# Optimization experiments

Hardware: AMD Instinct MI355X
Metric: run time of the kernel (lower is better)

The kernel has to match this reference:

```python
import jax, jax.numpy as jnp
import numpy as np

D_MODEL = 1024
NUM_HEADS = 16
D_K = D_MODEL // NUM_HEADS


def setup_inputs() -> dict:
    key = jax.random.key(0)
    ks = jax.random.split(key, 7)
    B, S = 4, 2048
    lim = float(np.sqrt(6.0 / (D_MODEL + D_MODEL)))  # xavier uniform
    x = jax.random.normal(ks[0], (B, S, D_MODEL), dtype=jnp.float32)
    w_q = jax.random.uniform(ks[1], (D_MODEL, D_MODEL), jnp.float32, -lim, lim)
    w_k = jax.random.uniform(ks[2], (D_MODEL, D_MODEL), jnp.float32, -lim, lim)
    w_v = jax.random.uniform(ks[3], (D_MODEL, D_MODEL), jnp.float32, -lim, lim)
    w_o = jax.random.uniform(ks[4], (D_MODEL, D_MODEL), jnp.float32, -lim, lim)
    b_o = jnp.zeros((D_MODEL,), jnp.float32)
    ln_g = jnp.ones((D_MODEL,), jnp.float32)
    ln_b = jnp.zeros((D_MODEL,), jnp.float32)
    return {"x": x, "w_q": w_q, "w_k": w_k, "w_v": w_v, "w_o": w_o,
            "b_o": b_o, "ln_g": ln_g, "ln_b": ln_b}


def _layer_norm(y, g, b, eps=1e-5):
    mu = jnp.mean(y, axis=-1, keepdims=True)
    var = jnp.var(y, axis=-1, keepdims=True)
    return (y - mu) * jax.lax.rsqrt(var + eps) * g + b


def reference(x, w_q, w_k, w_v, w_o, b_o, ln_g, ln_b):
    B, S, D = x.shape
    # Linear weights stored torch-style [out, in]: y = x @ W^T
    def proj(w):
        return jnp.einsum('bsd,ed->bse', x, w).reshape(B, S, NUM_HEADS, D_K).transpose(0, 2, 1, 3)
    Q, K, V = proj(w_q), proj(w_k), proj(w_v)  # [B, H, S, d_k]
    scores = jnp.einsum('bhqd,bhkd->bhqk', Q, K) / jnp.sqrt(jnp.float32(D_K))
    attn = jax.nn.softmax(scores, axis=-1)  # dropout identity at eval
    out = jnp.einsum('bhqk,bhkd->bhqd', attn, V)  # [B, H, S, d_k]
    out = out.transpose(0, 2, 1, 3).reshape(B, S, D)
    out = jnp.einsum('bsd,ed->bse', out, w_o) + b_o
    return _layer_norm(x + out, ln_g, ln_b)
```

## Files before the change

### kernel.cpp

```cpp
#include <hip/hip_runtime.h>

typedef __bf16 bf16;
typedef bf16 v8bf __attribute__((ext_vector_type(8)));
typedef bf16 v4bf __attribute__((ext_vector_type(4)));
typedef float v4f __attribute__((ext_vector_type(4)));

#define GAS __attribute__((address_space(1)))
#define LAS __attribute__((address_space(3)))

constexpr int D    = 1024;
constexpr int ROWS = 8192;
constexpr int TILE = 128;
constexpr int BK   = 32;

__global__ __launch_bounds__(256) void cast_f32_bf16(
    const float* __restrict__ in, bf16* __restrict__ out, int n4)
{
    int i = blockIdx.x * 256 + threadIdx.x;
    if (i < n4) {
        float4 v = ((const float4*)in)[i];
        v4bf o;
        o[0] = (bf16)v.x; o[1] = (bf16)v.y; o[2] = (bf16)v.z; o[3] = (bf16)v.w;
        ((v4bf*)out)[i] = o;
    }
}

template<int MODE>
__global__ __launch_bounds__(256) void gemm_bt(
    const bf16* __restrict__ A,
    const bf16* __restrict__ W0, const bf16* __restrict__ W1, const bf16* __restrict__ W2,
    bf16* __restrict__ O0, bf16* __restrict__ O1, bf16* __restrict__ O2,
    float* __restrict__ Of, const float* __restrict__ bias,
    const float* __restrict__ X)
{
    __shared__ bf16 As[TILE * BK];
    __shared__ bf16 Bs[TILE * BK];

    const int tid  = threadIdx.x;
    const int lane = tid & 63;
    const int wave = tid >> 6;
    const int quad = lane >> 4;
    const int l16  = lane & 15;
    const int wm   = (wave >> 1) * 64;
    const int wn   = (wave & 1) * 64;

    const int z = blockIdx.z;
    const bf16* Bw = (MODE == 0) ? ((z == 0) ? W0 : ((z == 1) ? W1 : W2)) : W0;
    bf16*       Ob = (MODE == 0) ? ((z == 0) ? O0 : ((z == 1) ? O1 : O2)) : O0;

    const long rowA0 = (long)blockIdx.y * TILE;
    const long rowB0 = (long)blockIdx.x * TILE;

    const int stRow = wave * 16 + (lane >> 2);
    const int stCol = (lane & 3) * 8;
    const bf16* gA = A  + (rowA0 + stRow) * D + stCol;
    const bf16* gB = Bw + (rowB0 + stRow) * D + stCol;
    const int ldsOff = wave * 16 * BK;

    const v4f vzero = {0.f, 0.f, 0.f, 0.f};
    v4f acc[4][4];
    #pragma unroll
    for (int i = 0; i < 4; i++)
        #pragma unroll
        for (int j = 0; j < 4; j++) acc[i][j] = vzero;

    for (int k0 = 0; k0 < D; k0 += BK) {
        __syncthreads();
        #pragma unroll
        for (int i = 0; i < 2; ++i) {
            __builtin_amdgcn_global_load_lds((const GAS void*)(gA + (long)i * 64 * D),
                                             (LAS void*)(As + ldsOff + i * 64 * BK), 16, 0, 0);
            __builtin_amdgcn_global_load_lds((const GAS void*)(gB + (long)i * 64 * D),
                                             (LAS void*)(Bs + ldsOff + i * 64 * BK), 16, 0, 0);
        }
        gA += BK; gB += BK;
        __syncthreads();

        v8bf a[4], b[4];
        #pragma unroll
        for (int mi = 0; mi < 4; mi++)
            a[mi] = *(const v8bf*)(As + (wm + mi * 16 + l16) * BK + quad * 8);
        #pragma unroll
        for (int ni = 0; ni < 4; ni++)
            b[ni] = *(const v8bf*)(Bs + (wn + ni * 16 + l16) * BK + quad * 8);
        #pragma unroll
        for (int mi = 0; mi < 4; mi++)
            #pragma unroll
            for (int ni = 0; ni < 4; ni++)
                acc[mi][ni] = __builtin_amdgcn_mfma_f32_16x16x32_bf16(a[mi], b[ni], acc[mi][ni], 0, 0, 0);
    }

    const float qscale = 0.125f * 1.44269504f;

    if (MODE == 0 && z == 2) {
        #pragma unroll
        for (int mi = 0; mi < 4; mi++) {
            #pragma unroll
            for (int ni = 0; ni < 4; ni++) {
                const long col = rowB0 + wn + ni * 16 + l16;
                const long h_ = col >> 6, dd = col & 63;
                const long row0 = rowA0 + wm + mi * 16 + quad * 4;
                const long b_ = row0 >> 11, s0 = row0 & 2047;
                v4bf pk;
                #pragma unroll
                for (int r = 0; r < 4; r++) pk[r] = (bf16)acc[mi][ni][r];
                *(v4bf*)(Ob + ((b_ * 16 + h_) * 64 + dd) * 2048 + s0) = pk;
            }
        }
    } else {
        #pragma unroll
        for (int mi = 0; mi < 4; mi++) {
            #pragma unroll
            for (int ni = 0; ni < 4; ni++) {
                const long col = rowB0 + wn + ni * 16 + l16;
                float bv = (MODE == 1) ? bias[col] : 0.f;
                #pragma unroll
                for (int r = 0; r < 4; r++) {
                    const long row = rowA0 + wm + mi * 16 + quad * 4 + r;
                    float v = acc[mi][ni][r];
                    if (MODE == 1) Of[row * D + col] = v + bv + X[row * D + col];
                    else {
                        if (z == 0) v *= qscale;
                        Ob[row * D + col] = (bf16)v;
                    }
                }
            }
        }
    }
}

__global__ __launch_bounds__(256) void attn_kernel(
    const bf16* __restrict__ Q, const bf16* __restrict__ Kg,
    const bf16* __restrict__ VtG, bf16* __restrict__ O)
{
    const int qt = blockIdx.x, h = blockIdx.y, b = blockIdx.z;
    const int tid  = threadIdx.x;
    const int lane = tid & 63;
    const int wave = tid >> 6;
    const int quad = lane >> 4;
    const int l16  = lane & 15;

    __shared__ bf16 Kt[64 * 72];
    __shared__ bf16 Vt[64 * 72];
    __shared__ bf16 Ps[4][32 * 72];

    v8bf qB[2][2];
    #pragma unroll
    for (int qf = 0; qf < 2; qf++) {
        const long qrow = (long)(b * 2048 + qt * 128 + wave * 32 + qf * 16 + l16);
        #pragma unroll
        for (int hh = 0; hh < 2; hh++)
            qB[qf][hh] = *(const v8bf*)(Q + qrow * D + h * 64 + hh * 32 + quad * 8);
    }

    float l_acc[2] = {0.f, 0.f};
    v4f o_acc[2][4];
    const v4f vzero = {0.f, 0.f, 0.f, 0.f};
    #pragma unroll
    for (int qf = 0; qf < 2; qf++)
        #pragma unroll
        for (int nf = 0; nf < 4; nf++) o_acc[qf][nf] = vzero;

    const int sC = (tid & 7) * 8;
    const int iR = tid >> 3;
    const bf16* kBase = Kg + (long)b * 2048 * D + h * 64 + sC;
    const bf16* vBase = VtG + (long)(b * 16 + h) * 64 * 2048 + sC;

    v8bf kpre[2], vpre[2];
    #pragma unroll
    for (int rep = 0; rep < 2; ++rep) {
        const int i = rep * 32 + iR;
        kpre[rep] = *(const v8bf*)(kBase + (long)i * D);
        vpre[rep] = *(const v8bf*)(vBase + (long)i * 2048);
    }

    for (int kt = 0; kt < 32; ++kt) {
        __syncthreads();
        #pragma unroll
        for (int rep = 0; rep < 2; ++rep) {
            const int i = rep * 32 + iR;
            *(v8bf*)(Kt + i * 72 + sC) = kpre[rep];
            *(v8bf*)(Vt + i * 72 + sC) = vpre[rep];
        }
        __syncthreads();

        if (kt + 1 < 32) {
            #pragma unroll
            for (int rep = 0; rep < 2; ++rep) {
                const int i = rep * 32 + iR;
                kpre[rep] = *(const v8bf*)(kBase + (long)((kt + 1) * 64 + i) * D);
                vpre[rep] = *(const v8bf*)(vBase + (long)i * 2048 + (kt + 1) * 64);
            }
        }

        v4f st[4][2];
        #pragma unroll
        for (int kf = 0; kf < 4; kf++) {
            v8bf kA0 = *(const v8bf*)(Kt + (kf * 16 + l16) * 72 + quad * 8);
            v8bf kA1 = *(const v8bf*)(Kt + (kf * 16 + l16) * 72 + 32 + quad * 8);
            #pragma unroll
            for (int qf = 0; qf < 2; qf++) {
                v4f t = vzero;
                t = __builtin_amdgcn_mfma_f32_16x16x32_bf16(kA0, qB[qf][0], t, 0, 0, 0);
                t = __builtin_amdgcn_mfma_f32_16x16x32_bf16(kA1, qB[qf][1], t, 0, 0, 0);
                st[kf][qf] = t;
            }
        }

        #pragma unroll
        for (int qf = 0; qf < 2; qf++)
            #pragma unroll
            for (int kf = 0; kf < 4; kf++) {
                v4bf pk;
                #pragma unroll
                for (int r = 0; r < 4; r++) {
                    float p = exp2f(st[kf][qf][r]);
                    l_acc[qf] += p;
                    pk[r] = (bf16)p;
                }
                *(v4bf*)(&Ps[wave][(qf * 16 + l16) * 72 + kf * 16 + quad * 4]) = pk;
            }

        #pragma unroll
        for (int ks = 0; ks < 2; ++ks) {
            v8bf vb[4];
            #pragma unroll
            for (int nf = 0; nf < 4; nf++)
                vb[nf] = *(const v8bf*)(Vt + (nf * 16 + l16) * 72 + ks * 32 + quad * 8);
            #pragma unroll
            for (int qf = 0; qf < 2; qf++) {
                v8bf pa = *(const v8bf*)(&Ps[wave][(qf * 16 + l16) * 72 + ks * 32 + quad * 8]);
                #pragma unroll
                for (int nf = 0; nf < 4; nf++)
                    o_acc[qf][nf] = __builtin_amdgcn_mfma_f32_16x16x32_bf16(pa, vb[nf], o_acc[qf][nf], 0, 0, 0);
            }
        }
    }

    #pragma unroll
    for (int qf = 0; qf < 2; qf++) {
        float l = l_acc[qf];
        l += __shfl_xor(l, 16);
        l += __shfl_xor(l, 32);
        l_acc[qf] = l;
    }

    #pragma unroll
    for (int qf = 0; qf < 2; qf++) {
        float inv[4];
        #pragma unroll
        for (int r = 0; r < 4; r++) {
            const int src = (quad << 4) | (quad * 4 + r);
            inv[r] = 1.f / __shfl(l_acc[qf], src);
        }
        const long orow = (long)(b * 2048 + qt * 128 + wave * 32 + qf * 16 + quad * 4);
        #pragma unroll
        for (int nf = 0; nf < 4; nf++)
            #pragma unroll
            for (int r = 0; r < 4; r++)
                O[(orow + r) * D + h * 64 + nf * 16 + l16] = (bf16)(o_acc[qf][nf][r] * inv[r]);
    }
}

__global__ __launch_bounds__(256) void ln_kernel(
    const float* __restrict__ g, const float* __restrict__ beta,
    float* __restrict__ out)
{
    const int row = blockIdx.x;
    const int t = threadIdx.x;
    const int lane = t & 63, wave = t >> 6;
    const long base = (long)row * D + t * 4;

    float4 yv = *(const float4*)(out + base);
    float y0 = yv.x, y1 = yv.y, y2 = yv.z, y3 = yv.w;
    float s1 = y0 + y1 + y2 + y3;
    float s2 = y0*y0 + y1*y1 + y2*y2 + y3*y3;
    #pragma unroll
    for (int off = 1; off < 64; off <<= 1) {
        s1 += __shfl_xor(s1, off);
        s2 += __shfl_xor(s2, off);
    }
    __shared__ float r1[4], r2[4];
    if (lane == 0) { r1[wave] = s1; r2[wave] = s2; }
    __syncthreads();
    float S1 = r1[0] + r1[1] + r1[2] + r1[3];
    float S2 = r2[0] + r2[1] + r2[2] + r2[3];
    float mu  = S1 * (1.f / 1024.f);
    float var = S2 * (1.f / 1024.f) - mu * mu;
    float rsd = rsqrtf(var + 1e-5f);

    float4 gv = *(const float4*)(g + t * 4);
    float4 bv = *(const float4*)(beta + t * 4);
    float4 o;
    o.x = (y0 - mu) * rsd * gv.x + bv.x;
    o.y = (y1 - mu) * rsd * gv.y + bv.y;
    o.z = (y2 - mu) * rsd * gv.z + bv.z;
    o.w = (y3 - mu) * rsd * gv.w + bv.w;
    *(float4*)(out + base) = o;
}

extern "C" void kernel_launch(void* const* d_in, const int* in_sizes, int n_in,
                              void* d_out, int out_size, void* d_ws, size_t ws_size,
                              hipStream_t stream)
{
    const float* x   = (const float*)d_in[0];
    const float* wq  = (const float*)d_in[1];
    const float* wk  = (const float*)d_in[2];
    const float* wv  = (const float*)d_in[3];
    const float* wo  = (const float*)d_in[4];
    const float* bo  = (const float*)d_in[5];
    const float* lng = (const float*)d_in[6];
    const float* lnb = (const float*)d_in[7];
    float* out = (float*)d_out;

    char* ws = (char*)d_ws;
    bf16* xb  = (bf16*)(ws);
    bf16* wqb = (bf16*)(ws + (size_t)16 * 1024 * 1024);
    bf16* wkb = wqb + 1024 * 1024;
    bf16* wvb = wkb + 1024 * 1024;
    bf16* wob = wvb + 1024 * 1024;
    bf16* Qb  = (bf16*)(ws + (size_t)24 * 1024 * 1024);
    bf16* Kb  = Qb + (size_t)ROWS * D;
    bf16* VtG = Kb + (size_t)ROWS * D;
    bf16* Ab  = VtG + (size_t)ROWS * D;

    cast_f32_bf16<<<8192, 256, 0, stream>>>(x,  xb,  ROWS * D / 4);
    cast_f32_bf16<<<1024, 256, 0, stream>>>(wq, wqb, D * D / 4);
    cast_f32_bf16<<<1024, 256, 0, stream>>>(wk, wkb, D * D / 4);
    cast_f32_bf16<<<1024, 256, 0, stream>>>(wv, wvb, D * D / 4);
    cast_f32_bf16<<<1024, 256, 0, stream>>>(wo, wob, D * D / 4);

    dim3 gqkv(D / TILE, ROWS / TILE, 3);
    gemm_bt<0><<<gqkv, 256, 0, stream>>>(xb, wqb, wkb, wvb, Qb, Kb, VtG,
                                         nullptr, nullptr, nullptr);

    attn_kernel<<<dim3(16, 16, 4), 256, 0, stream>>>(Qb, Kb, VtG, Ab);

    dim3 gout(D / TILE, ROWS / TILE, 1);
    gemm_bt<1><<<gout, 256, 0, stream>>>(Ab, wob, nullptr, nullptr,
                                         nullptr, nullptr, nullptr, out, bo, x);

    ln_kernel<<<8192, 256, 0, stream>>>(lng, lnb, out);
}
```

Before: 335.6 us.

## Merge cast kernels, double GEMM k-step to 64, simplify attention load addressing

Five separate f32-to-bf16 cast launches are merged into one kernel that picks its source and destination by index range, removing four launches. The GEMM now loads two 32-wide K slices per iteration into two LDS buffers, halving the number of barrier pairs over the K loop at the cost of twice the LDS. The attention kernel's K/V prefetch addressing is rewritten with incrementing per-lane pointers in place of recomputed indices, trimming integer address arithmetic.

Result: faster. 328.2 us (-2.2%).

```diff
diff --git a/kernel.cpp b/kernel.cpp
--- a/kernel.cpp
+++ b/kernel.cpp
@@ -11,18 +11,28 @@
 constexpr int D    = 1024;
 constexpr int ROWS = 8192;
 constexpr int TILE = 128;
-constexpr int BK   = 32;
-
-__global__ __launch_bounds__(256) void cast_f32_bf16(
-    const float* __restrict__ in, bf16* __restrict__ out, int n4)
+
+__global__ __launch_bounds__(256) void cast_all(
+    const float* __restrict__ x,
+    const float* __restrict__ wq, const float* __restrict__ wk,
+    const float* __restrict__ wv, const float* __restrict__ wo,
+    bf16* __restrict__ xb, bf16* __restrict__ wqb, bf16* __restrict__ wkb,
+    bf16* __restrict__ wvb, bf16* __restrict__ wob)
 {
     int i = blockIdx.x * 256 + threadIdx.x;
-    if (i < n4) {
-        float4 v = ((const float4*)in)[i];
-        v4bf o;
-        o[0] = (bf16)v.x; o[1] = (bf16)v.y; o[2] = (bf16)v.z; o[3] = (bf16)v.w;
-        ((v4bf*)out)[i] = o;
-    }
+    const float* src; bf16* dst; int off;
+    if (i < 2 * 1024 * 1024) { src = x; dst = xb; off = i; }
+    else {
+        int j = i - 2 * 1024 * 1024;
+        int w = j >> 18;
+        off = j & ((1 << 18) - 1);
+        src = (w == 0) ? wq : (w == 1) ? wk : (w == 2) ? wv : wo;
+        dst = (w == 0) ? wqb : (w == 1) ? wkb : (w == 2) ? wvb : wob;
+    }
+    float4 v = ((const float4*)src)[off];
+    v4bf o;
+    o[0] = (bf16)v.x; o[1] = (bf16)v.y; o[2] = (bf16)v.z; o[3] = (bf16)v.w;
+    ((v4bf*)dst)[off] = o;
 }
 
 template<int MODE>
@@ -33,8 +43,8 @@
     float* __restrict__ Of, const float* __restrict__ bias,
     const float* __restrict__ X)
 {
-    __shared__ bf16 As[TILE * BK];
-    __shared__ bf16 Bs[TILE * BK];
+    __shared__ bf16 As[2][TILE * 32];
+    __shared__ bf16 Bs[2][TILE * 32];
 
     const int tid  = threadIdx.x;
     const int lane = tid & 63;
@@ -55,7 +65,7 @@
     const int stCol = (lane & 3) * 8;
     const bf16* gA = A  + (rowA0 + stRow) * D + stCol;
     const bf16* gB = Bw + (rowB0 + stRow) * D + stCol;
-    const int ldsOff = wave * 16 * BK;
+    const int ldsOff = wave * 16 * 32;
 
     const v4f vzero = {0.f, 0.f, 0.f, 0.f};
     v4f acc[4][4];
@@ -64,30 +74,37 @@
         #pragma unroll
         for (int j = 0; j < 4; j++) acc[i][j] = vzero;
 
-    for (int k0 = 0; k0 < D; k0 += BK) {
+    for (int k0 = 0; k0 < D; k0 += 64) {
         __syncthreads();
         #pragma unroll
-        for (int i = 0; i < 2; ++i) {
-            __builtin_amdgcn_global_load_lds((const GAS void*)(gA + (long)i * 64 * D),
-                                             (LAS void*)(As + ldsOff + i * 64 * BK), 16, 0, 0);
-            __builtin_amdgcn_global_load_lds((const GAS void*)(gB + (long)i * 64 * D),
-                                             (LAS void*)(Bs + ldsOff + i * 64 * BK), 16, 0, 0);
-        }
-        gA += BK; gB += BK;
+        for (int p = 0; p < 2; ++p)
+            #pragma unroll
+            for (int i = 0; i < 2; ++i) {
+                __builtin_amdgcn_global_load_lds(
+                    (const GAS void*)(gA + (long)i * 64 * D + p * 32),
+                    (LAS void*)(&As[p][ldsOff + i * 64 * 32]), 16, 0, 0);
+                __builtin_amdgcn_global_load_lds(
+                    (const GAS void*)(gB + (long)i * 64 * D + p * 32),
+                    (LAS void*)(&Bs[p][ldsOff + i * 64 * 32]), 16, 0, 0);
+            }
+        gA += 64; gB += 64;
         __syncthreads();
 
-        v8bf a[4], b[4];
-        #pragma unroll
-        for (int mi = 0; mi < 4; mi++)
-            a[mi] = *(const v8bf*)(As + (wm + mi * 16 + l16) * BK + quad * 8);
-        #pragma unroll
-        for (int ni = 0; ni < 4; ni++)
-            b[ni] = *(const v8bf*)(Bs + (wn + ni * 16 + l16) * BK + quad * 8);
-        #pragma unroll
-        for (int mi = 0; mi < 4; mi++)
+        #pragma unroll
+        for (int p = 0; p < 2; ++p) {
+            v8bf a[4], b[4];
+            #pragma unroll
+            for (int mi = 0; mi < 4; mi++)
+                a[mi] = *(const v8bf*)(&As[p][(wm + mi * 16 + l16) * 32 + quad * 8]);
             #pragma unroll
             for (int ni = 0; ni < 4; ni++)
-                acc[mi][ni] = __builtin_amdgcn_mfma_f32_16x16x32_bf16(a[mi], b[ni], acc[mi][ni], 0, 0, 0);
+                b[ni] = *(const v8bf*)(&Bs[p][(wn + ni * 16 + l16) * 32 + quad * 8]);
+            #pragma unroll
+            for (int mi = 0; mi < 4; mi++)
+                #pragma unroll
+                for (int ni = 0; ni < 4; ni++)
+                    acc[mi][ni] = __builtin_amdgcn_mfma_f32_16x16x32_bf16(a[mi], b[ni], acc[mi][ni], 0, 0, 0);
+        }
     }
 
     const float qscale = 0.125f * 1.44269504f;
@@ -163,34 +180,35 @@
 
     const int sC = (tid & 7) * 8;
     const int iR = tid >> 3;
-    const bf16* kBase = Kg + (long)b * 2048 * D + h * 64 + sC;
-    const bf16* vBase = VtG + (long)(b * 16 + h) * 64 * 2048 + sC;
+
+    const bf16* kLane = Kg  + (long)b * 2048 * D + h * 64 + sC + (long)iR * D;
+    const bf16* vLane = VtG + (long)(b * 16 + h) * 64 * 2048 + sC + (long)iR * 2048;
+    bf16* ktW = Kt + iR * 72 + sC;
+    bf16* vtW = Vt + iR * 72 + sC;
 
     v8bf kpre[2], vpre[2];
-    #pragma unroll
-    for (int rep = 0; rep < 2; ++rep) {
-        const int i = rep * 32 + iR;
-        kpre[rep] = *(const v8bf*)(kBase + (long)i * D);
-        vpre[rep] = *(const v8bf*)(vBase + (long)i * 2048);
-    }
+    kpre[0] = *(const v8bf*)(kLane);
+    kpre[1] = *(const v8bf*)(kLane + 32 * D);
+    vpre[0] = *(const v8bf*)(vLane);
+    vpre[1] = *(const v8bf*)(vLane + 32 * 2048);
+    kLane += 64 * D;
+    vLane += 64;
 
     for (int kt = 0; kt < 32; ++kt) {
         __syncthreads();
-        #pragma unroll
-        for (int rep = 0; rep < 2; ++rep) {
-            const int i = rep * 32 + iR;
-            *(v8bf*)(Kt + i * 72 + sC) = kpre[rep];
-            *(v8bf*)(Vt + i * 72 + sC) = vpre[rep];
-        }
+        *(v8bf*)(ktW)            = kpre[0];
+        *(v8bf*)(ktW + 32 * 72)  = kpre[1];
+        *(v8bf*)(vtW)            = vpre[0];
+        *(v8bf*)(vtW + 32 * 72)  = vpre[1];
         __syncthreads();
 
         if (kt + 1 < 32) {
-            #pragma unroll
-            for (int rep = 0; rep < 2; ++rep) {
-                const int i = rep * 32 + iR;
-                kpre[rep] = *(const v8bf*)(kBase + (long)((kt + 1) * 64 + i) * D);
-                vpre[rep] = *(const v8bf*)(vBase + (long)i * 2048 + (kt + 1) * 64);
-            }
+            kpre[0] = *(const v8bf*)(kLane);
+            kpre[1] = *(const v8bf*)(kLane + 32 * D);
+            vpre[0] = *(const v8bf*)(vLane);
+            vpre[1] = *(const v8bf*)(vLane + 32 * 2048);
+            kLane += 64 * D;
+            vLane += 64;
         }
 
         v4f st[4][2];
@@ -324,11 +342,8 @@
     bf16* VtG = Kb + (size_t)ROWS * D;
     bf16* Ab  = VtG + (size_t)ROWS * D;
 
-    cast_f32_bf16<<<8192, 256, 0, stream>>>(x,  xb,  ROWS * D / 4);
-    cast_f32_bf16<<<1024, 256, 0, stream>>>(wq, wqb, D * D / 4);
-    cast_f32_bf16<<<1024, 256, 0, stream>>>(wk, wkb, D * D / 4);
-    cast_f32_bf16<<<1024, 256, 0, stream>>>(wv, wvb, D * D / 4);
-    cast_f32_bf16<<<1024, 256, 0, stream>>>(wo, wob, D * D / 4);
+    cast_all<<<12288, 256, 0, stream>>>(x, wq, wk, wv, wo,
+                                        xb, wqb, wkb, wvb, wob);
 
     dim3 gqkv(D / TILE, ROWS / TILE, 3);
     gemm_bt<0><<<gqkv, 256, 0, stream>>>(xb, wqb, wkb, wvb, Qb, Kb, VtG,
```
